# Performance work log

Measured on AMD Instinct MI355X. Metric: run time of the kernel, lower is better.

## Reference

```python
import jax, jax.numpy as jnp
import numpy as np

B, T, S = 64, 128, 512
E, H = 256, 512
GRU_IN = E + 2 * H  # 1280


def setup_inputs() -> dict:
    key = jax.random.key(0)
    ks = jax.random.split(key, 12)
    sc = 0.02
    return {
        "trg_embed": jax.random.normal(ks[0], (B, T, E), jnp.float32),
        "enc_hidden": jax.random.normal(ks[1], (B, S, 2 * H), jnp.float32),
        "enc_final": jax.random.normal(ks[2], (1, B, 2 * H), jnp.float32),
        "data_mask": jnp.ones((B, 1, S), jnp.int32),
        # attention params
        "W_key": jax.random.normal(ks[3], (H, 2 * H), jnp.float32) * sc,
        "W_query": jax.random.normal(ks[4], (H, H), jnp.float32) * sc,
        "w_energy": jax.random.normal(ks[5], (H,), jnp.float32) * sc,
        # bridge
        "W_bridge": jax.random.normal(ks[6], (H, 2 * H), jnp.float32) * sc,
        "b_bridge": jnp.zeros((H,), jnp.float32),
        # GRU (single layer, batch_first)
        "W_ih": jax.random.normal(ks[7], (3 * H, GRU_IN), jnp.float32) * sc,
        "W_hh": jax.random.normal(ks[8], (3 * H, H), jnp.float32) * sc,
        "b_ih": jnp.zeros((3 * H,), jnp.float32),
        "b_hh": jnp.zeros((3 * H,), jnp.float32),
        # pre_out: Linear(H + 2H + E -> H, bias=False)
        "W_pre": jax.random.normal(ks[9], (H, H + 2 * H + E), jnp.float32) * sc,
    }


def _decode(trg_embed, enc_hidden, enc_final, data_mask,
            W_key, W_query, w_energy, W_bridge, b_bridge,
            W_ih, W_hh, b_ih, b_hh, W_pre):
    # bridge: initial hidden state [B, H]
    h0 = jnp.tanh(enc_final[0] @ W_bridge.T + b_bridge)
    # precompute attention keys [B, S, H]
    proj_key = jnp.einsum('bsk,hk->bsh', enc_hidden, W_key)
    mask = data_mask[:, 0, :] != 0  # [B, S]

    def step(h, x_t):  # h: [B,H], x_t: [B,E]
        # Bahdanau attention
        q = x_t_query = h @ W_query.T                      # [B, H]
        e = jnp.einsum('bsh,h->bs', jnp.tanh(q[:, None, :] + proj_key), w_energy)  # [B,S]
        e = jnp.where(mask, e, -1e9)
        alphas = jax.nn.softmax(e, axis=-1)                # [B, S]
        context = jnp.einsum('bs,bsd->bd', alphas, enc_hidden)  # [B, 2H]
        # GRU cell
        x = jnp.concatenate([x_t, context], axis=-1)       # [B, E+2H]
        gx = x @ W_ih.T + b_ih                             # [B, 3H]
        gh = h @ W_hh.T + b_hh                             # [B, 3H]
        rx, zx, nx = jnp.split(gx, 3, axis=-1)
        rh, zh, nh = jnp.split(gh, 3, axis=-1)
        r = jax.nn.sigmoid(rx + rh)
        z = jax.nn.sigmoid(zx + zh)
        n = jnp.tanh(nx + r * nh)
        h_new = (1.0 - z) * n + z * h                      # [B, H]
        # pre-output projection
        pre = jnp.concatenate([x_t, h_new, context], axis=-1) @ W_pre.T  # [B, H]
        return h_new, (h_new, pre)

    xs = jnp.transpose(trg_embed, (1, 0, 2))  # [T, B, E]
    h_last, (states, pre_outs) = jax.lax.scan(step, h0, xs)
    decoder_states = jnp.transpose(states, (1, 0, 2))      # [B, T, H]
    pre_output_vectors = jnp.transpose(pre_outs, (1, 0, 2))  # [B, T, H]
    hidden = h_last[None]                                  # [1, B, H]
    return decoder_states, hidden, pre_output_vectors


def reference(trg_embed, enc_hidden, enc_final, data_mask,
              W_key, W_query, w_energy, W_bridge, b_bridge,
              W_ih, W_hh, b_ih, b_hh, W_pre):
    return _decode(trg_embed, enc_hidden, enc_final, data_mask,
                   W_key, W_query, w_energy, W_bridge, b_bridge,
                   W_ih, W_hh, b_ih, b_hh, W_pre)
```

## Files before the change

kernel.cpp:

```cpp
#include <hip/hip_runtime.h>


#define LDSS 40

typedef short bf16x8 __attribute__((ext_vector_type(8)));
typedef float f32x4 __attribute__((ext_vector_type(4)));

__device__ inline ushort f2b(float f) {
    unsigned int u = __float_as_uint(f);
    return (ushort)((u + 0x7FFFu + ((u >> 16) & 1u)) >> 16);
}
__device__ inline float b2f(ushort u) {
    return __uint_as_float(((unsigned int)u) << 16);
}
__device__ inline float fast_tanh(float x) {
    x = fminf(fmaxf(x, -15.f), 15.f);
    float ex = __expf(2.f * x);
    return (ex - 1.f) / (ex + 1.f);
}

__global__ void f2b4_kernel(const float4* __restrict__ in, ushort4* __restrict__ out, int n4) {
    int i = blockIdx.x * blockDim.x + threadIdx.x;
    int stride = gridDim.x * blockDim.x;
    for (; i < n4; i += stride) {
        float4 v = in[i];
        ushort4 o;
        o.x = f2b(v.x); o.y = f2b(v.y); o.z = f2b(v.z); o.w = f2b(v.w);
        out[i] = o;
    }
}

template <bool AF32, bool ATOMIC>
__device__ inline void gemm64x64(const void* __restrict__ Av,
                                 const ushort* __restrict__ B,
                                 ushort* As, ushort* Bs,
                                 int lda, int ldb, int kbeg, int kend,
                                 float* Cf, ushort* Cb, long ldc,
                                 long m0, long n0)
{
    const int tid  = threadIdx.x;
    const int wave = tid >> 6;
    const int lane = tid & 63;
    const int row  = tid >> 2;
    const int kcol = (tid & 3) * 8;
    const int lrow = lane & 15;
    const int quad = lane >> 4;

    f32x4 acc[4];
#pragma unroll
    for (int i = 0; i < 4; i++) acc[i] = f32x4{0.f, 0.f, 0.f, 0.f};

    const ushort* Ab  = (const ushort*)Av + (m0 + row) * (long)lda + kcol;
    const float*  Afp = (const float*)Av + (m0 + row) * (long)lda + kcol;
    const ushort* Bp  = B + (n0 + row) * (long)ldb + kcol;
    ushort* AsW = As + row * LDSS + kcol;
    ushort* BsW = Bs + row * LDSS + kcol;
    const ushort* AsR = As + (wave * 16 + lrow) * LDSS + quad * 8;
    const ushort* BsR = Bs + lrow * LDSS + quad * 8;

    for (int k0 = kbeg; k0 < kend; k0 += 32) {
        uint4 av;
        if (AF32) {
            float4 f0 = *(const float4*)(Afp + k0);
            float4 f1 = *(const float4*)(Afp + k0 + 4);
            av.x = (uint)f2b(f0.x) | ((uint)f2b(f0.y) << 16);
            av.y = (uint)f2b(f0.z) | ((uint)f2b(f0.w) << 16);
            av.z = (uint)f2b(f1.x) | ((uint)f2b(f1.y) << 16);
            av.w = (uint)f2b(f1.z) | ((uint)f2b(f1.w) << 16);
        } else {
            av = *(const uint4*)(Ab + k0);
        }
        uint4 bv = *(const uint4*)(Bp + k0);
        __syncthreads();
        *(uint4*)AsW = av;
        *(uint4*)BsW = bv;
        __syncthreads();
        bf16x8 af = *(const bf16x8*)AsR;
#pragma unroll
        for (int nf = 0; nf < 4; nf++) {
            bf16x8 bfv = *(const bf16x8*)(BsR + nf * 16 * LDSS);
            acc[nf] = __builtin_amdgcn_mfma_f32_16x16x32_bf16(af, bfv, acc[nf], 0, 0, 0);
        }
    }

#pragma unroll
    for (int nf = 0; nf < 4; nf++) {
#pragma unroll
        for (int r = 0; r < 4; r++) {
            long m = m0 + wave * 16 + quad * 4 + r;
            long n = n0 + nf * 16 + lrow;
            float v = acc[nf][r];
            if (ATOMIC)      atomicAdd(&Cf[m * ldc + n], v);
            else if (Cf)     Cf[m * ldc + n] = v;
            else             Cb[m * ldc + n] = f2b(v);
        }
    }
}

template <bool AF32>
__global__ void gemm_nt(const void* __restrict__ A, const ushort* __restrict__ B,
                        float* Cf, ushort* Cb,
                        int lda, int ldb, long ldc, int K, int nTilesN)
{
    __shared__ ushort As[64 * LDSS];
    __shared__ ushort Bs[64 * LDSS];
    long m0 = (long)(blockIdx.x / nTilesN) * 64;
    long n0 = (long)(blockIdx.x % nTilesN) * 64;
    gemm64x64<AF32, false>(A, B, As, Bs, lda, ldb, 0, K, Cf, Cb, ldc, m0, n0);
}

__global__ void stepA_kernel(const ushort* __restrict__ h_b,
                             const ushort* __restrict__ cat2,
                             const ushort* __restrict__ Wq,
                             const ushort* __restrict__ Whh,
                             const ushort* __restrict__ Wpre,
                             float* q, float* gh, float* pre_out, int t)
{
    __shared__ ushort As[64 * LDSS];
    __shared__ ushort Bs[64 * LDSS];
    int bid = blockIdx.x;
    if (bid < 32) {
        if (t == 0) return;
        int kc = bid >> 3, nt = bid & 7;
        gemm64x64<false, true>(cat2, Wpre, As, Bs, 1792, 1792, kc * 448, kc * 448 + 448,
                               pre_out + (long)(t - 1) * 512, nullptr, 65536, 0, (long)nt * 64);
    } else if (bid < 48) {
        int b2 = bid - 32, kc = b2 >> 3, nt = b2 & 7;
        gemm64x64<false, true>(h_b, Wq, As, Bs, 512, 512, kc * 256, kc * 256 + 256,
                               q, nullptr, 512, 0, (long)nt * 64);
    } else {
        int b3 = bid - 48, kc = b3 / 24, nt = b3 % 24;
        gemm64x64<false, true>(h_b, Whh, As, Bs, 512, 512, kc * 256, kc * 256 + 256,
                               gh, nullptr, 1536, 0, (long)nt * 64);
    }
}

__global__ void gx_kernel(const ushort* __restrict__ xcat, const ushort* __restrict__ Wih,
                          float* gx)
{
    __shared__ ushort As[64 * LDSS];
    __shared__ ushort Bs[64 * LDSS];
    int nt = blockIdx.x % 24, kc = blockIdx.x / 24;
    gemm64x64<false, true>(xcat, Wih, As, Bs, 1280, 1280, kc * 320, kc * 320 + 320,
                           gx, nullptr, 1536, 0, (long)nt * 64);
}

__global__ void e_kernel(const ushort* __restrict__ pk, const float* __restrict__ q,
                         const float* __restrict__ wE, const int* __restrict__ mask,
                         float* __restrict__ e)
{
    int wid  = (blockIdx.x * blockDim.x + threadIdx.x) >> 6;
    int lane = threadIdx.x & 63;
    int b = wid >> 9, s = wid & 511;
    const ushort* pkp = pk + ((long)(b * 512 + s) << 9) + lane * 8;
    const float*  qp  = q + ((long)b << 9) + lane * 8;
    const float*  wp  = wE + lane * 8;
    bf16x8 pv = *(const bf16x8*)pkp;
    float4 q0 = *(const float4*)qp, q1 = *(const float4*)(qp + 4);
    float4 w0 = *(const float4*)wp, w1 = *(const float4*)(wp + 4);
    float acc;
    acc  = fast_tanh(q0.x + b2f((ushort)pv[0])) * w0.x;
    acc += fast_tanh(q0.y + b2f((ushort)pv[1])) * w0.y;
    acc += fast_tanh(q0.z + b2f((ushort)pv[2])) * w0.z;
    acc += fast_tanh(q0.w + b2f((ushort)pv[3])) * w0.w;
    acc += fast_tanh(q1.x + b2f((ushort)pv[4])) * w1.x;
    acc += fast_tanh(q1.y + b2f((ushort)pv[5])) * w1.y;
    acc += fast_tanh(q1.z + b2f((ushort)pv[6])) * w1.z;
    acc += fast_tanh(q1.w + b2f((ushort)pv[7])) * w1.w;
#pragma unroll
    for (int off = 32; off; off >>= 1) acc += __shfl_xor(acc, off);
    if (lane == 0) {
        int i = (b << 9) + s;
        e[i] = (mask[i] != 0) ? acc : -1e9f;
    }
}

__global__ void sc_kernel(const float* __restrict__ e,
                          const float* __restrict__ encf, const ushort* __restrict__ encb,
                          int useb, const float* __restrict__ trg,
                          ushort* __restrict__ xcat, ushort* __restrict__ cat2, int t)
{
    __shared__ float alpha[512];
    __shared__ float red[256];
    __shared__ float part[256];
    int b  = blockIdx.x >> 4;
    int dc = blockIdx.x & 15;
    int tid = threadIdx.x;
    float p0 = __expf(e[(b << 9) + tid]);
    float p1 = __expf(e[(b << 9) + 256 + tid]);
    alpha[tid] = p0;
    alpha[tid + 256] = p1;
    red[tid] = p0 + p1;
    __syncthreads();
    for (int off = 128; off; off >>= 1) {
        if (tid < off) red[tid] += red[tid + off];
        __syncthreads();
    }
    float inv = 1.f / red[0];
    int dl = tid & 63;
    int sr = tid >> 6;
    int d  = (dc << 6) + dl;
    float a0 = 0.f, a1 = 0.f, a2 = 0.f, a3 = 0.f;
    if (useb) {
        const ushort* p = encb + ((long)b << 19) + d;
        for (int s = sr; s < 512; s += 16) {
            a0 += alpha[s]      * b2f(p[(long)s << 10]);
            a1 += alpha[s + 4]  * b2f(p[(long)(s + 4) << 10]);
            a2 += alpha[s + 8]  * b2f(p[(long)(s + 8) << 10]);
            a3 += alpha[s + 12] * b2f(p[(long)(s + 12) << 10]);
        }
    } else {
        const float* p = encf + ((long)b << 19) + d;
        for (int s = sr; s < 512; s += 16) {
            a0 += alpha[s]      * p[(long)s << 10];
            a1 += alpha[s + 4]  * p[(long)(s + 4) << 10];
            a2 += alpha[s + 8]  * p[(long)(s + 8) << 10];
            a3 += alpha[s + 12] * p[(long)(s + 12) << 10];
        }
    }
    part[tid] = ((a0 + a1) + (a2 + a3));
    __syncthreads();
    if (sr == 0) {
        float ctx = (part[dl] + part[64 + dl] + part[128 + dl] + part[192 + dl]) * inv;
        ushort cb = f2b(ctx);
        xcat[b * 1280 + 256 + d] = cb;
        cat2[b * 1792 + 768 + d] = cb;
    } else if (sr == 1 && dc < 4) {
        ushort xv = f2b(trg[((long)b * 128 + t) * 256 + (dc << 6) + dl]);
        xcat[b * 1280 + (dc << 6) + dl] = xv;
        cat2[b * 1792 + (dc << 6) + dl] = xv;
    }
}

__global__ void gates_kernel(float* __restrict__ gx, float* __restrict__ gh,
                             const float* __restrict__ bih, const float* __restrict__ bhh,
                             float* __restrict__ h, ushort* __restrict__ h_b,
                             ushort* __restrict__ cat2, float* __restrict__ d_states,
                             float* __restrict__ q, float* __restrict__ out_pre, int t)
{
    int idx = blockIdx.x * blockDim.x + threadIdx.x;
    int b = idx >> 9, j = idx & 511;
    float* gxp = gx + b * 1536;
    float* ghp = gh + b * 1536;
    float rx = gxp[j]        + bih[j];
    float zx = gxp[j + 512]  + bih[j + 512];
    float nx = gxp[j + 1024] + bih[j + 1024];
    float rh = ghp[j]        + bhh[j];
    float zh = ghp[j + 512]  + bhh[j + 512];
    float nh = ghp[j + 1024] + bhh[j + 1024];
    float r = 1.f / (1.f + __expf(-(rx + rh)));
    float z = 1.f / (1.f + __expf(-(zx + zh)));
    float n = fast_tanh(nx + r * nh);
    float hn = (1.f - z) * n + z * h[idx];
    h[idx] = hn;
    h_b[idx] = f2b(hn);
    cat2[b * 1792 + 256 + j] = f2b(hn);
    d_states[((long)b * 128 + t) * 512 + j] = hn;
    gxp[j] = 0.f; gxp[j + 512] = 0.f; gxp[j + 1024] = 0.f;
    ghp[j] = 0.f; ghp[j + 512] = 0.f; ghp[j + 1024] = 0.f;
    q[idx] = 0.f;
    out_pre[((long)b * 128 + t) * 512 + j] = 0.f;
}

__global__ void btanh_kernel(const float* __restrict__ br, const float* __restrict__ bbr,
                             float* __restrict__ h, ushort* __restrict__ h_b,
                             float* __restrict__ q, float* __restrict__ gh,
                             float* __restrict__ gx)
{
    int idx = blockIdx.x * blockDim.x + threadIdx.x;
    int b = idx >> 9, j = idx & 511;
    float v = fast_tanh(br[idx] + bbr[j]);
    h[idx] = v;
    h_b[idx] = f2b(v);
    q[idx] = 0.f;
    gh[b * 1536 + j] = 0.f; gh[b * 1536 + j + 512] = 0.f; gh[b * 1536 + j + 1024] = 0.f;
    gx[b * 1536 + j] = 0.f; gx[b * 1536 + j + 512] = 0.f; gx[b * 1536 + j + 1024] = 0.f;
}

__global__ void hid_kernel(const float* __restrict__ h, float* __restrict__ out)
{
    int idx = blockIdx.x * blockDim.x + threadIdx.x;
    out[idx] = h[idx];
}

extern "C" void kernel_launch(void* const* d_in, const int* in_sizes, int n_in,
                              void* d_out, int out_size, void* d_ws, size_t ws_size,
                              hipStream_t stream)
{
    (void)in_sizes; (void)n_in; (void)out_size;
    const float* trg  = (const float*)d_in[0];
    const float* enc  = (const float*)d_in[1];
    const float* encF = (const float*)d_in[2];
    const int*   mask = (const int*)d_in[3];
    const float* Wkey = (const float*)d_in[4];
    const float* Wq   = (const float*)d_in[5];
    const float* wE   = (const float*)d_in[6];
    const float* Wbr  = (const float*)d_in[7];
    const float* bbr  = (const float*)d_in[8];
    const float* Wih  = (const float*)d_in[9];
    const float* Whh  = (const float*)d_in[10];
    const float* bih  = (const float*)d_in[11];
    const float* bhh  = (const float*)d_in[12];
    const float* Wpre = (const float*)d_in[13];

    char* p = (char*)d_ws;
    auto alloc = [&](size_t bytes) { void* r = (void*)p; p += (bytes + 255) & ~(size_t)255; return r; };
    ushort* pk     = (ushort*)alloc(16777216ul * 2);
    ushort* Wkey_b = (ushort*)alloc(524288ul * 2);
    ushort* Wq_b   = (ushort*)alloc(262144ul * 2);
    ushort* Wbr_b  = (ushort*)alloc(524288ul * 2);
    ushort* Wih_b  = (ushort*)alloc(1966080ul * 2);
    ushort* Whh_b  = (ushort*)alloc(786432ul * 2);
    ushort* Wpre_b = (ushort*)alloc(917504ul * 2);
    float*  h    = (float*)alloc(32768ul * 4);
    ushort* h_b  = (ushort*)alloc(32768ul * 2);
    float*  br   = (float*)alloc(32768ul * 4);
    float*  q    = (float*)alloc(32768ul * 4);
    float*  gh   = (float*)alloc(98304ul * 4);
    float*  gx   = (float*)alloc(98304ul * 4);
    float*  e    = (float*)alloc(32768ul * 4);
    ushort* xcat = (ushort*)alloc(81920ul * 2);
    ushort* cat2 = (ushort*)alloc(114688ul * 2);
    size_t used = (size_t)(p - (char*)d_ws);
    int useb = (used + 33554432ul * 2 <= ws_size) ? 1 : 0;
    ushort* enc_b = useb ? (ushort*)alloc(33554432ul * 2) : nullptr;

    float* out_states = (float*)d_out;
    float* out_hidden = out_states + 64l * 128 * 512;
    float* out_pre    = out_hidden + 64l * 512;

    f2b4_kernel<<<512, 256, 0, stream>>>((const float4*)Wkey, (ushort4*)Wkey_b, 131072);
    f2b4_kernel<<<256, 256, 0, stream>>>((const float4*)Wq,   (ushort4*)Wq_b,   65536);
    f2b4_kernel<<<512, 256, 0, stream>>>((const float4*)Wbr,  (ushort4*)Wbr_b,  131072);
    f2b4_kernel<<<1920, 256, 0, stream>>>((const float4*)Wih, (ushort4*)Wih_b,  491520);
    f2b4_kernel<<<768, 256, 0, stream>>>((const float4*)Whh,  (ushort4*)Whh_b,  196608);
    f2b4_kernel<<<896, 256, 0, stream>>>((const float4*)Wpre, (ushort4*)Wpre_b, 229376);

    if (useb) {
        f2b4_kernel<<<8192, 256, 0, stream>>>((const float4*)enc, (ushort4*)enc_b, 8388608);
        gemm_nt<false><<<4096, 256, 0, stream>>>(enc_b, Wkey_b, nullptr, pk, 1024, 1024, 512, 1024, 8);
    } else {
        gemm_nt<true><<<4096, 256, 0, stream>>>(enc, Wkey_b, nullptr, pk, 1024, 1024, 512, 1024, 8);
    }
    gemm_nt<true><<<8, 256, 0, stream>>>(encF, Wbr_b, br, nullptr, 1024, 1024, 512, 1024, 8);
    btanh_kernel<<<128, 256, 0, stream>>>(br, bbr, h, h_b, q, gh, gx);

    for (int t = 0; t < 128; t++) {
        stepA_kernel<<<96, 256, 0, stream>>>(h_b, cat2, Wq_b, Whh_b, Wpre_b, q, gh, out_pre, t);
        e_kernel<<<8192, 256, 0, stream>>>(pk, q, wE, mask, e);
        sc_kernel<<<1024, 256, 0, stream>>>(e, enc, enc_b, useb, trg, xcat, cat2, t);
        gx_kernel<<<96, 256, 0, stream>>>(xcat, Wih_b, gx);
        gates_kernel<<<128, 256, 0, stream>>>(gx, gh, bih, bhh, h, h_b, cat2, out_states,
                                              q, out_pre, t);
    }
    stepA_kernel<<<32, 256, 0, stream>>>(h_b, cat2, Wq_b, Whh_b, Wpre_b, q, gh, out_pre, 128);
    hid_kernel<<<128, 256, 0, stream>>>(h, out_hidden);
}
```

Measured before the change: 6.036 ms.

## Fuse context reduction with input-gate projection and transpose encoder for coalesced reads

The encoder states are transposed once into a bf16 [B, 2H, S] layout, so the per-step attention-weighted context sum reads contiguous vectors instead of strided scalars. The separate gx GEMM kernel is removed. Each context block now multiplies its 64-wide context slice (and its embedding slice) against the matching W_ih columns and accumulates into gx with atomics, which saves one kernel launch per step. The cost is that every one of the 1024 blocks reads a 1536x64 slice of W_ih with scalar FMAs and issues many float atomics, replacing a small MFMA GEMM. The key projection now reads fp32 encoder states directly rather than a pre-converted bf16 copy.

```diff
diff --git a/kernel.cpp b/kernel.cpp
--- a/kernel.cpp
+++ b/kernel.cpp
@@ -27,6 +27,31 @@
         ushort4 o;
         o.x = f2b(v.x); o.y = f2b(v.y); o.z = f2b(v.z); o.w = f2b(v.w);
         out[i] = o;
+    }
+}
+
+__global__ void tr_kernel(const float* __restrict__ enc, ushort* __restrict__ et)
+{
+    __shared__ ushort lds[64][68];
+    int bid = blockIdx.x;
+    int b  = bid >> 7;
+    int dt = (bid >> 3) & 15;
+    int st = bid & 7;
+    int tid = threadIdx.x;
+    long base = ((long)b * 512 + st * 64) * 1024 + dt * 64;
+#pragma unroll
+    for (int i = 0; i < 16; i++) {
+        int s = (tid >> 6) + (i << 2);
+        int d = tid & 63;
+        lds[d][s] = f2b(enc[base + (long)s * 1024 + d]);
+    }
+    __syncthreads();
+    long obase = ((long)b * 1024 + dt * 64) * 512 + st * 64;
+#pragma unroll
+    for (int i = 0; i < 16; i++) {
+        int d = (tid >> 6) + (i << 2);
+        int s = tid & 63;
+        et[obase + (long)d * 512 + s] = lds[d][s];
     }
 }
 
@@ -133,16 +158,6 @@
         gemm64x64<false, true>(h_b, Whh, As, Bs, 512, 512, kc * 256, kc * 256 + 256,
                                gh, nullptr, 1536, 0, (long)nt * 64);
     }
-}
-
-__global__ void gx_kernel(const ushort* __restrict__ xcat, const ushort* __restrict__ Wih,
-                          float* gx)
-{
-    __shared__ ushort As[64 * LDSS];
-    __shared__ ushort Bs[64 * LDSS];
-    int nt = blockIdx.x % 24, kc = blockIdx.x / 24;
-    gemm64x64<false, true>(xcat, Wih, As, Bs, 1280, 1280, kc * 320, kc * 320 + 320,
-                           gx, nullptr, 1536, 0, (long)nt * 64);
 }
 
 __global__ void e_kernel(const ushort* __restrict__ pk, const float* __restrict__ q,
@@ -175,60 +190,121 @@
     }
 }
 
-__global__ void sc_kernel(const float* __restrict__ e,
-                          const float* __restrict__ encf, const ushort* __restrict__ encb,
-                          int useb, const float* __restrict__ trg,
-                          ushort* __restrict__ xcat, ushort* __restrict__ cat2, int t)
+__global__ void sc2_kernel(const float* __restrict__ e,
+                           const float* __restrict__ encf, const ushort* __restrict__ enc_t,
+                           int useb, const float* __restrict__ trg,
+                           const ushort* __restrict__ Wih,
+                           ushort* __restrict__ cat2, float* __restrict__ gx, int t)
 {
     __shared__ float alpha[512];
-    __shared__ float red[256];
+    __shared__ float wred[4];
+    __shared__ float ctxs[64];
+    __shared__ float xts[64];
     __shared__ float part[256];
     int b  = blockIdx.x >> 4;
     int dc = blockIdx.x & 15;
     int tid = threadIdx.x;
+    int lane = tid & 63;
     float p0 = __expf(e[(b << 9) + tid]);
     float p1 = __expf(e[(b << 9) + 256 + tid]);
-    alpha[tid] = p0;
-    alpha[tid + 256] = p1;
-    red[tid] = p0 + p1;
+    alpha[tid] = p0; alpha[tid + 256] = p1;
+    float wsum = p0 + p1;
+#pragma unroll
+    for (int off = 32; off; off >>= 1) wsum += __shfl_xor(wsum, off);
+    if (lane == 0) wred[tid >> 6] = wsum;
     __syncthreads();
-    for (int off = 128; off; off >>= 1) {
-        if (tid < off) red[tid] += red[tid + off];
+    float inv = 1.f / (wred[0] + wred[1] + wred[2] + wred[3]);
+
+    if (useb) {
+        int d   = tid >> 2;
+        int qtr = tid & 3;
+        const ushort* pe = enc_t + (((long)b * 1024 + (dc << 6) + d) << 9) + (qtr << 7);
+        const float* al = alpha + (qtr << 7);
+        float acc = 0.f;
+#pragma unroll
+        for (int i = 0; i < 16; i++) {
+            bf16x8 v = *(const bf16x8*)(pe + i * 8);
+            acc += al[i*8+0] * b2f((ushort)v[0]) + al[i*8+1] * b2f((ushort)v[1])
+                 + al[i*8+2] * b2f((ushort)v[2]) + al[i*8+3] * b2f((ushort)v[3])
+                 + al[i*8+4] * b2f((ushort)v[4]) + al[i*8+5] * b2f((ushort)v[5])
+                 + al[i*8+6] * b2f((ushort)v[6]) + al[i*8+7] * b2f((ushort)v[7]);
+        }
+        acc += __shfl_xor(acc, 1);
+        acc += __shfl_xor(acc, 2);
+        if (qtr == 0) {
+            ushort cb = f2b(acc * inv);
+            cat2[b * 1792 + 768 + (dc << 6) + d] = cb;
+            ctxs[d] = b2f(cb);
+        }
+        if (dc < 4 && tid < 64) {
+            ushort xv = f2b(trg[((long)b * 128 + t) * 256 + (dc << 6) + tid]);
+            cat2[b * 1792 + (dc << 6) + tid] = xv;
+            xts[tid] = b2f(xv);
+        }
+    } else {
+        int dl = lane, sr = tid >> 6;
+        int d = (dc << 6) + dl;
+        const float* pf = encf + ((long)b << 19) + d;
+        float a0 = 0.f, a1 = 0.f, a2 = 0.f, a3 = 0.f;
+        for (int s = sr; s < 512; s += 16) {
+            a0 += alpha[s]      * pf[(long)s << 10];
+            a1 += alpha[s + 4]  * pf[(long)(s + 4) << 10];
+            a2 += alpha[s + 8]  * pf[(long)(s + 8) << 10];
+            a3 += alpha[s + 12] * pf[(long)(s + 12) << 10];
+        }
+        part[tid] = (a0 + a1) + (a2 + a3);
         __syncthreads();
-    }
-    float inv = 1.f / red[0];
-    int dl = tid & 63;
-    int sr = tid >> 6;
-    int d  = (dc << 6) + dl;
-    float a0 = 0.f, a1 = 0.f, a2 = 0.f, a3 = 0.f;
-    if (useb) {
-        const ushort* p = encb + ((long)b << 19) + d;
-        for (int s = sr; s < 512; s += 16) {
-            a0 += alpha[s]      * b2f(p[(long)s << 10]);
-            a1 += alpha[s + 4]  * b2f(p[(long)(s + 4) << 10]);
-            a2 += alpha[s + 8]  * b2f(p[(long)(s + 8) << 10]);
-            a3 += alpha[s + 12] * b2f(p[(long)(s + 12) << 10]);
-        }
-    } else {
-        const float* p = encf + ((long)b << 19) + d;
-        for (int s = sr; s < 512; s += 16) {
-            a0 += alpha[s]      * p[(long)s << 10];
-            a1 += alpha[s + 4]  * p[(long)(s + 4) << 10];
-            a2 += alpha[s + 8]  * p[(long)(s + 8) << 10];
-            a3 += alpha[s + 12] * p[(long)(s + 12) << 10];
-        }
-    }
-    part[tid] = ((a0 + a1) + (a2 + a3));
+        if (sr == 0) {
+            float ctx = (part[dl] + part[64 + dl] + part[128 + dl] + part[192 + dl]) * inv;
+            ushort cb = f2b(ctx);
+            cat2[b * 1792 + 768 + d] = cb;
+            ctxs[dl] = b2f(cb);
+        } else if (sr == 1 && dc < 4) {
+            ushort xv = f2b(trg[((long)b * 128 + t) * 256 + (dc << 6) + dl]);
+            cat2[b * 1792 + (dc << 6) + dl] = xv;
+            xts[dl] = b2f(xv);
+        }
+    }
     __syncthreads();
-    if (sr == 0) {
-        float ctx = (part[dl] + part[64 + dl] + part[128 + dl] + part[192 + dl]) * inv;
-        ushort cb = f2b(ctx);
-        xcat[b * 1280 + 256 + d] = cb;
-        cat2[b * 1792 + 768 + d] = cb;
-    } else if (sr == 1 && dc < 4) {
-        ushort xv = f2b(trg[((long)b * 128 + t) * 256 + (dc << 6) + dl]);
-        xcat[b * 1280 + (dc << 6) + dl] = xv;
-        cat2[b * 1792 + (dc << 6) + dl] = xv;
+
+    {
+        float* gxb = gx + b * 1536;
+        const ushort* wbase = Wih + 256 + (dc << 6);
+#pragma unroll
+        for (int j = 0; j < 6; j++) {
+            int col = tid * 6 + j;
+            const ushort* wr = wbase + (long)col * 1280;
+            float acc = 0.f;
+#pragma unroll
+            for (int g = 0; g < 8; g++) {
+                bf16x8 wv = *(const bf16x8*)(wr + g * 8);
+                const float* cs = ctxs + g * 8;
+                acc += cs[0]*b2f((ushort)wv[0]) + cs[1]*b2f((ushort)wv[1])
+                     + cs[2]*b2f((ushort)wv[2]) + cs[3]*b2f((ushort)wv[3])
+                     + cs[4]*b2f((ushort)wv[4]) + cs[5]*b2f((ushort)wv[5])
+                     + cs[6]*b2f((ushort)wv[6]) + cs[7]*b2f((ushort)wv[7]);
+            }
+            atomicAdd(&gxb[col], acc);
+        }
+        if (dc < 4) {
+            const ushort* wbase2 = Wih + (dc << 6);
+#pragma unroll
+            for (int j = 0; j < 6; j++) {
+                int col = tid * 6 + j;
+                const ushort* wr = wbase2 + (long)col * 1280;
+                float acc = 0.f;
+#pragma unroll
+                for (int g = 0; g < 8; g++) {
+                    bf16x8 wv = *(const bf16x8*)(wr + g * 8);
+                    const float* cs = xts + g * 8;
+                    acc += cs[0]*b2f((ushort)wv[0]) + cs[1]*b2f((ushort)wv[1])
+                         + cs[2]*b2f((ushort)wv[2]) + cs[3]*b2f((ushort)wv[3])
+                         + cs[4]*b2f((ushort)wv[4]) + cs[5]*b2f((ushort)wv[5])
+                         + cs[6]*b2f((ushort)wv[6]) + cs[7]*b2f((ushort)wv[7]);
+                }
+                atomicAdd(&gxb[col], acc);
+            }
+        }
     }
 }
 
@@ -319,11 +395,10 @@
     float*  gh   = (float*)alloc(98304ul * 4);
     float*  gx   = (float*)alloc(98304ul * 4);
     float*  e    = (float*)alloc(32768ul * 4);
-    ushort* xcat = (ushort*)alloc(81920ul * 2);
     ushort* cat2 = (ushort*)alloc(114688ul * 2);
     size_t used = (size_t)(p - (char*)d_ws);
     int useb = (used + 33554432ul * 2 <= ws_size) ? 1 : 0;
-    ushort* enc_b = useb ? (ushort*)alloc(33554432ul * 2) : nullptr;
+    ushort* enc_t = useb ? (ushort*)alloc(33554432ul * 2) : nullptr;
 
     float* out_states = (float*)d_out;
     float* out_hidden = out_states + 64l * 128 * 512;
@@ -336,20 +411,16 @@
     f2b4_kernel<<<768, 256, 0, stream>>>((const float4*)Whh,  (ushort4*)Whh_b,  196608);
     f2b4_kernel<<<896, 256, 0, stream>>>((const float4*)Wpre, (ushort4*)Wpre_b, 229376);
 
-    if (useb) {
-        f2b4_kernel<<<8192, 256, 0, stream>>>((const float4*)enc, (ushort4*)enc_b, 8388608);
-        gemm_nt<false><<<4096, 256, 0, stream>>>(enc_b, Wkey_b, nullptr, pk, 1024, 1024, 512, 1024, 8);
-    } else {
-        gemm_nt<true><<<4096, 256, 0, stream>>>(enc, Wkey_b, nullptr, pk, 1024, 1024, 512, 1024, 8);
-    }
+    gemm_nt<true><<<4096, 256, 0, stream>>>(enc, Wkey_b, nullptr, pk, 1024, 1024, 512, 1024, 8);
+    if (useb) tr_kernel<<<8192, 256, 0, stream>>>(enc, enc_t);
+
     gemm_nt<true><<<8, 256, 0, stream>>>(encF, Wbr_b, br, nullptr, 1024, 1024, 512, 1024, 8);
     btanh_kernel<<<128, 256, 0, stream>>>(br, bbr, h, h_b, q, gh, gx);
 
     for (int t = 0; t < 128; t++) {
         stepA_kernel<<<96, 256, 0, stream>>>(h_b, cat2, Wq_b, Whh_b, Wpre_b, q, gh, out_pre, t);
         e_kernel<<<8192, 256, 0, stream>>>(pk, q, wE, mask, e);
-        sc_kernel<<<1024, 256, 0, stream>>>(e, enc, enc_b, useb, trg, xcat, cat2, t);
-        gx_kernel<<<96, 256, 0, stream>>>(xcat, Wih_b, gx);
+        sc2_kernel<<<1024, 256, 0, stream>>>(e, enc, enc_t, useb, trg, Wih_b, cat2, gx, t);
         gates_kernel<<<128, 256, 0, stream>>>(gx, gh, bih, bhh, h, h_b, cat2, out_states,
                                               q, out_pre, t);
     }
```

New measurement: 17.26 ms. 186% more time.

## Regroup per-step GEMMs into q and gx/gh/pre kernels; double-buffer cat2

Applied to the files above, without the earlier changes.

Each step's launches are reorganised. The q GEMM now runs alone in a small kernel before attention. The W_hh, W_ih and previous-step pre-output GEMMs are merged into one 176-block kernel launched after the context is computed, which needs a double-buffered cat2 so the pre-output read of step t-1 does not collide with the write for step t. The energy kernel is also changed so each wave handles four source positions with software-prefetched loads, cutting its grid from 8192 to 2048 blocks. The trade-off is that the q GEMM no longer shares a launch with the other GEMMs, while the merged kernel fills more CUs.

```diff
diff --git a/kernel.cpp b/kernel.cpp
--- a/kernel.cpp
+++ b/kernel.cpp
@@ -109,12 +109,21 @@
     gemm64x64<AF32, false>(A, B, As, Bs, lda, ldb, 0, K, Cf, Cb, ldc, m0, n0);
 }
 
-__global__ void stepA_kernel(const ushort* __restrict__ h_b,
-                             const ushort* __restrict__ cat2,
-                             const ushort* __restrict__ Wq,
-                             const ushort* __restrict__ Whh,
-                             const ushort* __restrict__ Wpre,
-                             float* q, float* gh, float* pre_out, int t)
+__global__ void q_kernel(const ushort* __restrict__ h_b, const ushort* __restrict__ Wq,
+                         float* q)
+{
+    __shared__ ushort As[64 * LDSS];
+    __shared__ ushort Bs[64 * LDSS];
+    int kc = blockIdx.x >> 3, nt = blockIdx.x & 7;
+    gemm64x64<false, true>(h_b, Wq, As, Bs, 512, 512, kc * 256, kc * 256 + 256,
+                           q, nullptr, 512, 0, (long)nt * 64);
+}
+
+__global__ void gxgh_kernel(const ushort* __restrict__ xcat, const ushort* __restrict__ h_b,
+                            const ushort* __restrict__ cat2r,
+                            const ushort* __restrict__ Wih, const ushort* __restrict__ Whh,
+                            const ushort* __restrict__ Wpre,
+                            float* gx, float* gh, float* pre_out, int t)
 {
     __shared__ ushort As[64 * LDSS];
     __shared__ ushort Bs[64 * LDSS];
@@ -122,27 +131,17 @@
     if (bid < 32) {
         if (t == 0) return;
         int kc = bid >> 3, nt = bid & 7;
-        gemm64x64<false, true>(cat2, Wpre, As, Bs, 1792, 1792, kc * 448, kc * 448 + 448,
+        gemm64x64<false, true>(cat2r, Wpre, As, Bs, 1792, 1792, kc * 448, kc * 448 + 448,
                                pre_out + (long)(t - 1) * 512, nullptr, 65536, 0, (long)nt * 64);
-    } else if (bid < 48) {
-        int b2 = bid - 32, kc = b2 >> 3, nt = b2 & 7;
-        gemm64x64<false, true>(h_b, Wq, As, Bs, 512, 512, kc * 256, kc * 256 + 256,
-                               q, nullptr, 512, 0, (long)nt * 64);
-    } else {
-        int b3 = bid - 48, kc = b3 / 24, nt = b3 % 24;
+    } else if (bid < 80) {
+        int b3 = bid - 32, kc = b3 / 24, nt = b3 % 24;
         gemm64x64<false, true>(h_b, Whh, As, Bs, 512, 512, kc * 256, kc * 256 + 256,
                                gh, nullptr, 1536, 0, (long)nt * 64);
-    }
-}
-
-__global__ void gx_kernel(const ushort* __restrict__ xcat, const ushort* __restrict__ Wih,
-                          float* gx)
-{
-    __shared__ ushort As[64 * LDSS];
-    __shared__ ushort Bs[64 * LDSS];
-    int nt = blockIdx.x % 24, kc = blockIdx.x / 24;
-    gemm64x64<false, true>(xcat, Wih, As, Bs, 1280, 1280, kc * 320, kc * 320 + 320,
-                           gx, nullptr, 1536, 0, (long)nt * 64);
+    } else {
+        int b4 = bid - 80, nt = b4 % 24, kc = b4 / 24;
+        gemm64x64<false, true>(xcat, Wih, As, Bs, 1280, 1280, kc * 320, kc * 320 + 320,
+                               gx, nullptr, 1536, 0, (long)nt * 64);
+    }
 }
 
 __global__ void e_kernel(const ushort* __restrict__ pk, const float* __restrict__ q,
@@ -151,27 +150,34 @@
 {
     int wid  = (blockIdx.x * blockDim.x + threadIdx.x) >> 6;
     int lane = threadIdx.x & 63;
-    int b = wid >> 9, s = wid & 511;
-    const ushort* pkp = pk + ((long)(b * 512 + s) << 9) + lane * 8;
-    const float*  qp  = q + ((long)b << 9) + lane * 8;
-    const float*  wp  = wE + lane * 8;
-    bf16x8 pv = *(const bf16x8*)pkp;
+    int b  = wid >> 7;
+    int s0 = (wid & 127) << 2;
+    const float* qp = q + ((long)b << 9) + lane * 8;
+    const float* wp = wE + lane * 8;
     float4 q0 = *(const float4*)qp, q1 = *(const float4*)(qp + 4);
     float4 w0 = *(const float4*)wp, w1 = *(const float4*)(wp + 4);
-    float acc;
-    acc  = fast_tanh(q0.x + b2f((ushort)pv[0])) * w0.x;
-    acc += fast_tanh(q0.y + b2f((ushort)pv[1])) * w0.y;
-    acc += fast_tanh(q0.z + b2f((ushort)pv[2])) * w0.z;
-    acc += fast_tanh(q0.w + b2f((ushort)pv[3])) * w0.w;
-    acc += fast_tanh(q1.x + b2f((ushort)pv[4])) * w1.x;
-    acc += fast_tanh(q1.y + b2f((ushort)pv[5])) * w1.y;
-    acc += fast_tanh(q1.z + b2f((ushort)pv[6])) * w1.z;
-    acc += fast_tanh(q1.w + b2f((ushort)pv[7])) * w1.w;
-#pragma unroll
-    for (int off = 32; off; off >>= 1) acc += __shfl_xor(acc, off);
-    if (lane == 0) {
-        int i = (b << 9) + s;
-        e[i] = (mask[i] != 0) ? acc : -1e9f;
+    const ushort* pkb = pk + (((long)(b << 9) + s0) << 9) + lane * 8;
+    bf16x8 pv = *(const bf16x8*)pkb;
+#pragma unroll
+    for (int j = 0; j < 4; j++) {
+        bf16x8 pn;
+        if (j < 3) pn = *(const bf16x8*)(pkb + ((long)(j + 1) << 9));
+        float acc;
+        acc  = fast_tanh(q0.x + b2f((ushort)pv[0])) * w0.x;
+        acc += fast_tanh(q0.y + b2f((ushort)pv[1])) * w0.y;
+        acc += fast_tanh(q0.z + b2f((ushort)pv[2])) * w0.z;
+        acc += fast_tanh(q0.w + b2f((ushort)pv[3])) * w0.w;
+        acc += fast_tanh(q1.x + b2f((ushort)pv[4])) * w1.x;
+        acc += fast_tanh(q1.y + b2f((ushort)pv[5])) * w1.y;
+        acc += fast_tanh(q1.z + b2f((ushort)pv[6])) * w1.z;
+        acc += fast_tanh(q1.w + b2f((ushort)pv[7])) * w1.w;
+#pragma unroll
+        for (int off = 32; off; off >>= 1) acc += __shfl_xor(acc, off);
+        if (lane == 0) {
+            int i = (b << 9) + s0 + j;
+            e[i] = (mask[i] != 0) ? acc : -1e9f;
+        }
+        pv = pn;
     }
 }
 
@@ -320,7 +326,7 @@
     float*  gx   = (float*)alloc(98304ul * 4);
     float*  e    = (float*)alloc(32768ul * 4);
     ushort* xcat = (ushort*)alloc(81920ul * 2);
-    ushort* cat2 = (ushort*)alloc(114688ul * 2);
+    ushort* cat2 = (ushort*)alloc(229376ul * 2);
     size_t used = (size_t)(p - (char*)d_ws);
     int useb = (used + 33554432ul * 2 <= ws_size) ? 1 : 0;
     ushort* enc_b = useb ? (ushort*)alloc(33554432ul * 2) : nullptr;
@@ -346,13 +352,17 @@
     btanh_kernel<<<128, 256, 0, stream>>>(br, bbr, h, h_b, q, gh, gx);
 
     for (int t = 0; t < 128; t++) {
-        stepA_kernel<<<96, 256, 0, stream>>>(h_b, cat2, Wq_b, Whh_b, Wpre_b, q, gh, out_pre, t);
-        e_kernel<<<8192, 256, 0, stream>>>(pk, q, wE, mask, e);
-        sc_kernel<<<1024, 256, 0, stream>>>(e, enc, enc_b, useb, trg, xcat, cat2, t);
-        gx_kernel<<<96, 256, 0, stream>>>(xcat, Wih_b, gx);
-        gates_kernel<<<128, 256, 0, stream>>>(gx, gh, bih, bhh, h, h_b, cat2, out_states,
+        ushort* cat2w = cat2 + (size_t)(t & 1) * 114688;
+        ushort* cat2r = cat2 + (size_t)((t + 1) & 1) * 114688;
+        q_kernel<<<16, 256, 0, stream>>>(h_b, Wq_b, q);
+        e_kernel<<<2048, 256, 0, stream>>>(pk, q, wE, mask, e);
+        sc_kernel<<<1024, 256, 0, stream>>>(e, enc, enc_b, useb, trg, xcat, cat2w, t);
+        gxgh_kernel<<<176, 256, 0, stream>>>(xcat, h_b, cat2r, Wih_b, Whh_b, Wpre_b,
+                                             gx, gh, out_pre, t);
+        gates_kernel<<<128, 256, 0, stream>>>(gx, gh, bih, bhh, h, h_b, cat2w, out_states,
                                               q, out_pre, t);
     }
-    stepA_kernel<<<32, 256, 0, stream>>>(h_b, cat2, Wq_b, Whh_b, Wpre_b, q, gh, out_pre, 128);
+    gxgh_kernel<<<32, 256, 0, stream>>>(xcat, h_b, cat2 + 114688, Wih_b, Whh_b, Wpre_b,
+                                        gx, gh, out_pre, 128);
     hid_kernel<<<128, 256, 0, stream>>>(h, out_hidden);
 }
```

New measurement: 5.921 ms (median of 2 runs). Within noise of the previous version (-1.9%).
